# Optimization experiments

Measured on AMD Instinct MI355X. Metric: run time of the kernel, lower is better.

The kernel has to match this reference:

```python
import jax, jax.numpy as jnp
import numpy as np

HIDDEN = 4096
N_HEADS = 32
N_KV_HEADS = 8
HEAD_DIM = HIDDEN // N_HEADS  # 128
ROPE_THETA = 10000.0
NEG_INF = -1e9


def rotate_half(x):
    x1, x2 = jnp.split(x, 2, axis=-1)
    return jnp.concatenate([-x2, x1], axis=-1)


def rope_cos_sin(seq_len, dim, dtype):
    inv_freq = 1.0 / (ROPE_THETA ** (jnp.arange(0, dim, 2, dtype=jnp.float32) / dim))
    t = jnp.arange(seq_len, dtype=jnp.float32)
    freqs = jnp.outer(t, inv_freq)              # (S, dim/2)
    emb = jnp.concatenate([freqs, freqs], -1)   # (S, dim)
    return jnp.cos(emb).astype(dtype), jnp.sin(emb).astype(dtype)


def setup_inputs() -> dict:
    key = jax.random.key(0)
    ks = jax.random.split(key, 5)
    B, S = 2, 2048
    hidden_states = jax.random.normal(ks[0], (B, S, HIDDEN), jnp.float32)
    # additive causal mask (B, 1, S, S)
    causal = jnp.triu(jnp.full((S, S), NEG_INF, jnp.float32), k=1)
    attention_mask = jnp.broadcast_to(causal[None, None], (B, 1, S, S))
    scale = 0.02
    wq = jax.random.normal(ks[1], (HIDDEN, HIDDEN), jnp.float32) * scale
    wk = jax.random.normal(ks[2], (N_KV_HEADS * HEAD_DIM, HIDDEN), jnp.float32) * scale
    wv = jax.random.normal(ks[3], (N_KV_HEADS * HEAD_DIM, HIDDEN), jnp.float32) * scale
    wo = jax.random.normal(ks[4], (HIDDEN, HIDDEN), jnp.float32) * scale
    return {"hidden_states": hidden_states, "attention_mask": attention_mask,
            "wq": wq, "wk": wk, "wv": wv, "wo": wo}


def reference(hidden_states, attention_mask, wq, wk, wv, wo):
    B, S, _ = hidden_states.shape
    H, Hk, D = N_HEADS, N_KV_HEADS, HEAD_DIM
    G = H // Hk  # kv groups

    q = (hidden_states @ wq.T).reshape(B, S, H, D).transpose(0, 2, 1, 3)   # (B,H,S,D)
    k = (hidden_states @ wk.T).reshape(B, S, Hk, D).transpose(0, 2, 1, 3)  # (B,Hk,S,D)
    v = (hidden_states @ wv.T).reshape(B, S, Hk, D).transpose(0, 2, 1, 3)

    cos, sin = rope_cos_sin(S, D, hidden_states.dtype)  # (S,D)
    cos = cos[None, None]  # (1,1,S,D)
    sin = sin[None, None]
    q = q * cos + rotate_half(q) * sin
    k = k * cos + rotate_half(k) * sin

    # GQA without materializing repeated K/V: view q as (B,Hk,G,S,D)
    qg = q.reshape(B, Hk, G, S, D)
    scores = jnp.einsum('bkgqd,bkld->bkgql', qg, k) / jnp.sqrt(jnp.asarray(D, q.dtype))
    scores = scores + attention_mask[:, :, None]  # (B,1,1,S,S) broadcast
    attn = jax.nn.softmax(scores.astype(jnp.float32), axis=-1).astype(q.dtype)
    out = jnp.einsum('bkgql,bkld->bkgqd', attn, v)  # (B,Hk,G,S,D)
    out = out.reshape(B, H, S, D).transpose(0, 2, 1, 3).reshape(B, S, H * D)
    return out @ wo.T
```

## Files before the change

kernel.cpp:

```cpp
#include <hip/hip_runtime.h>
#include <hip/hip_bf16.h>
#include <stdint.h>


#define HIDDEN 4096
#define NH 32
#define NKV 8
#define HD 128
#define SLEN 2048
#define BATCH 2
#define QKVLD 6144

typedef __attribute__((ext_vector_type(8))) short bf16x8;
typedef __attribute__((ext_vector_type(4))) float f32x4;

__device__ __forceinline__ unsigned short f2bf(float f) {
  __hip_bfloat16 h = __float2bfloat16(f);
  return *reinterpret_cast<unsigned short*>(&h);
}
__device__ __forceinline__ float bf2f(unsigned short h) {
  union { uint32_t u; float f; } v; v.u = ((uint32_t)h) << 16;
  return v.f;
}
__device__ __forceinline__ void gload_lds16(const void* g, void* l) {
  __builtin_amdgcn_global_load_lds(
      (const __attribute__((address_space(1))) unsigned int*)g,
      (__attribute__((address_space(3))) unsigned int*)l, 16, 0, 0);
}

__device__ __forceinline__ void cvt_body(const float* __restrict__ in,
                                         unsigned short* __restrict__ out, int rb) {
  size_t i = ((size_t)rb * 256 + threadIdx.x) * 8;
  f32x4 a = *(const f32x4*)&in[i];
  f32x4 b = *(const f32x4*)&in[i + 4];
  bf16x8 o;
#pragma unroll
  for (int j = 0; j < 4; ++j) { o[j] = (short)f2bf(a[j]); o[4 + j] = (short)f2bf(b[j]); }
  *(bf16x8*)&out[i] = o;
}

__global__ __launch_bounds__(256) void cvt_f32_bf16(const float* __restrict__ in,
                                                    unsigned short* __restrict__ out) {
  cvt_body(in, out, blockIdx.x);
}

__global__ __launch_bounds__(256) void cvt_all(const float* __restrict__ h,
                                               const float* __restrict__ wq,
                                               const float* __restrict__ wk,
                                               const float* __restrict__ wv,
                                               unsigned short* __restrict__ Xbf,
                                               unsigned short* __restrict__ Wqkv) {
  int bid = blockIdx.x;
  if (bid < 8192) {
    cvt_body(h, Xbf, bid);
  } else if (bid < 16384) {
    cvt_body(wq, Wqkv, bid - 8192);
  } else if (bid < 18432) {
    cvt_body(wk, Wqkv + (size_t)4096 * 4096, bid - 16384);
  } else {
    cvt_body(wv, Wqkv + (size_t)5120 * 4096, bid - 18432);
  }
}

__device__ __forceinline__ void store_out(unsigned short* C, size_t i, float v) { C[i] = f2bf(v); }
__device__ __forceinline__ void store_out(float* C, size_t i, float v) { C[i] = v; }

template <typename OutT>
__global__ __launch_bounds__(512, 2)
void gemm_bt256(const unsigned short* __restrict__ A, const unsigned short* __restrict__ B,
                OutT* __restrict__ C, int M, int N, int K) {
  __shared__ __align__(16) unsigned short lds[4 * 2048 * 8];

  const int tid = threadIdx.x;
  const int lane = tid & 63, w = tid >> 6;
  const int lr = lane & 15, lg = lane >> 4;
  const int wr = w >> 2, wc = w & 3;
  const int rsw = (lr >> 1) & 3;

  const int nbn = N >> 8;
  const int nwg = gridDim.x;
  int wg = (int)blockIdx.x;
  wg = (wg & 7) * (nwg >> 3) + (wg >> 3);
  const int bm = wg / nbn, bn = wg % nbn;

  const unsigned short* Ab = A + (size_t)bm * 256 * K;
  const unsigned short* Bb = B + (size_t)bn * 256 * K;

  const int r0 = tid >> 2, s0 = (tid & 3) ^ ((tid >> 3) & 3);
  const int L1 = tid + 512;
  const int r1 = L1 >> 2, s1 = (L1 & 3) ^ ((L1 >> 3) & 3);
  const unsigned short* gA0 = Ab + (size_t)r0 * K + s0 * 8;
  const unsigned short* gA1 = Ab + (size_t)r1 * K + s1 * 8;
  const unsigned short* gB0 = Bb + (size_t)r0 * K + s0 * 8;
  const unsigned short* gB1 = Bb + (size_t)r1 * K + s1 * 8;

  const unsigned short* rdA = &lds[(size_t)(wr * 512 + lr * 4 + (lg ^ rsw)) * 8];
  const unsigned short* rdB = &lds[(size_t)(1024 + wc * 256 + lr * 4 + (lg ^ rsw)) * 8];

  f32x4 acc[8][4] = {};

  auto stage = [&](int t2) {
    unsigned short* lb = lds + (size_t)(t2 & 3) * 2048 * 8;
    const int off = t2 * 32;
    gload_lds16(gA0 + off, lb + (size_t)tid * 8);
    gload_lds16(gA1 + off, lb + (size_t)(512 + tid) * 8);
    gload_lds16(gB0 + off, lb + (size_t)(1024 + tid) * 8);
    gload_lds16(gB1 + off, lb + (size_t)(1536 + tid) * 8);
  };

#define READ12(af, bf, bsel)                                                      \
  {                                                                               \
    const unsigned short* pA_ = rdA + (size_t)(bsel)*16384;                       \
    const unsigned short* pB_ = rdB + (size_t)(bsel)*16384;                       \
    _Pragma("unroll") for (int mi_ = 0; mi_ < 8; ++mi_)                           \
        af[mi_] = *(const bf16x8*)(pA_ + mi_ * 512);                              \
    _Pragma("unroll") for (int ni_ = 0; ni_ < 4; ++ni_)                           \
        bf[ni_] = *(const bf16x8*)(pB_ + ni_ * 512);                              \
  }

#define MFMA32(af, bf)                                                            \
  __builtin_amdgcn_s_setprio(1);                                                  \
  _Pragma("unroll") for (int mi_ = 0; mi_ < 8; ++mi_)                             \
  _Pragma("unroll") for (int ni_ = 0; ni_ < 4; ++ni_)                             \
      acc[mi_][ni_] = __builtin_amdgcn_mfma_f32_16x16x32_bf16(                    \
          af[mi_], bf[ni_], acc[mi_][ni_], 0, 0, 0);                              \
  __builtin_amdgcn_s_setprio(0)

#define VMW(t)                                                                    \
  if ((t) + 3 < NT)      asm volatile("s_waitcnt vmcnt(8)" ::: "memory");         \
  else if ((t) + 2 < NT) asm volatile("s_waitcnt vmcnt(4)" ::: "memory");         \
  else if ((t) + 1 < NT) asm volatile("s_waitcnt vmcnt(0)" ::: "memory")

#define ITER(cur_a, cur_b, nxt_a, nxt_b, t)                                       \
  {                                                                               \
    if ((t) + 3 < NT) stage((t) + 3);                                             \
    VMW(t);                                                                       \
    __builtin_amdgcn_s_barrier();                                                 \
    if ((t) + 1 < NT) READ12(nxt_a, nxt_b, ((t) + 1) & 3);                        \
    MFMA32(cur_a, cur_b);                                                         \
    asm volatile("s_waitcnt lgkmcnt(0)" ::: "memory");                            \
  }

  const int NT = K >> 5;

  bf16x8 afA[8], bfA[4], afB[8], bfB[4];

  stage(0); stage(1); stage(2);
  asm volatile("s_waitcnt vmcnt(8)" ::: "memory");
  __builtin_amdgcn_s_barrier();
  READ12(afA, bfA, 0);

#pragma unroll 1
  for (int t = 0; t < NT; t += 2) {
    ITER(afA, bfA, afB, bfB, t);
    ITER(afB, bfB, afA, bfA, t + 1);
  }

#pragma unroll
  for (int mi = 0; mi < 8; ++mi)
#pragma unroll
    for (int ni = 0; ni < 4; ++ni)
#pragma unroll
      for (int r = 0; r < 4; ++r) {
        size_t row = (size_t)bm * 256 + wr * 128 + mi * 16 + lg * 4 + r;
        size_t col = (size_t)bn * 256 + wc * 64 + ni * 16 + lr;
        store_out(C, row * N + col, acc[mi][ni][r]);
      }
#undef READ12
#undef MFMA32
#undef VMW
#undef ITER
}

__global__ __launch_bounds__(256) void rope_tables(float* __restrict__ ct, float* __restrict__ st) {
  int idx = blockIdx.x * 256 + threadIdx.x;
  int s = idx >> 6, j = idx & 63;
  float inv = exp2f(-(float)j * (13.287712379549449f / 64.f));
  float f = (float)s * inv;
  ct[idx] = cosf(f);
  st[idx] = sinf(f);
}

__device__ __forceinline__ void rope_body(unsigned short* __restrict__ X, int ld,
                                          const float* __restrict__ ct,
                                          const float* __restrict__ st, int heads, int idx) {
  int jc = (idx & 7) * 8;
  int t2 = idx >> 3;
  int hh = t2 % heads;
  int row = t2 / heads;
  int s = row & (SLEN - 1);
  unsigned short* p = X + (size_t)row * ld + hh * HD;
  bf16x8 lo = *(bf16x8*)&p[jc];
  bf16x8 hi = *(bf16x8*)&p[64 + jc];
  bf16x8 nlo, nhi;
#pragma unroll
  for (int j = 0; j < 8; ++j) {
    float c = ct[s * 64 + jc + j];
    float sn = st[s * 64 + jc + j];
    float xl = bf2f((unsigned short)(lo[j]));
    float xh = bf2f((unsigned short)(hi[j]));
    nlo[j] = (short)f2bf(xl * c - xh * sn);
    nhi[j] = (short)f2bf(xh * c + xl * sn);
  }
  *(bf16x8*)&p[jc] = nlo;
  *(bf16x8*)&p[64 + jc] = nhi;
}

__global__ __launch_bounds__(256) void rope_apply_qk(unsigned short* __restrict__ QKV,
                                                     const float* __restrict__ ct,
                                                     const float* __restrict__ st) {
  int bid = blockIdx.x;
  if (bid < 4096) {
    rope_body(QKV, QKVLD, ct, st, NH, bid * 256 + threadIdx.x);
  } else {
    rope_body(QKV + 4096, QKVLD, ct, st, NKV, (bid - 4096) * 256 + threadIdx.x);
  }
}

__global__ __launch_bounds__(256) void transpose_v(const unsigned short* __restrict__ Vsrc, int ld,
                                                   unsigned short* __restrict__ VT) {
  __shared__ unsigned short tile[64][66];
  const int t = threadIdx.x;
  const int bs = blockIdx.x;
  const int bd = blockIdx.y;
  const int b = bs >> 5;
  const int s0 = (bs & 31) * 64;
  const int d0 = bd * 64;
#pragma unroll
  for (int it = 0; it < 2; ++it) {
    int si = (t >> 3) + it * 32;
    int dj = (t & 7) * 8;
    bf16x8 v = *(const bf16x8*)&Vsrc[(size_t)(b * SLEN + s0 + si) * ld + d0 + dj];
#pragma unroll
    for (int j = 0; j < 8; ++j) tile[si][dj + j] = (unsigned short)(v[j]);
  }
  __syncthreads();
#pragma unroll
  for (int it = 0; it < 2; ++it) {
    int di = (t >> 3) + it * 32;
    int sj = (t & 7) * 8;
    bf16x8 o;
#pragma unroll
    for (int j = 0; j < 8; ++j) o[j] = (short)tile[sj + j][di];
    int c = d0 + di;
    int kvh = c >> 7, d = c & 127;
    *(bf16x8*)&VT[(((size_t)b * NKV + kvh) * HD + d) * SLEN + s0 + sj] = o;
  }
}

__global__ __launch_bounds__(256, 2)
void attn_fwd(const unsigned short* __restrict__ QKV, const unsigned short* __restrict__ VTm,
              unsigned short* __restrict__ Om) {
  const int blk = blockIdx.x;
  const int xcd = blk & 7, jj = blk >> 3;
  const int g = xcd + ((jj >> 5) << 3);
  const int pair = jj & 31;
  const int kvh = g & 7, b = g >> 3;
  const int tid = threadIdx.x;
  const int lane = tid & 63, w = tid >> 6;
  const int lr = lane & 15, lg = lane >> 4;
  const int h = kvh * 4 + w;

  __shared__ __align__(16) unsigned short Ksm[64 * 136];
  __shared__ __align__(16) unsigned short Vsm[128 * 72];
  __shared__ __align__(16) unsigned short Psm[4][32 * 72];
  __shared__ float Alds[4][32];

  const float SL2E = 0.1275378504229740f;

  const unsigned short* Kb0 = QKV + (size_t)(b * SLEN) * QKVLD + 4096 + kvh * HD;
  const unsigned short* VTb = VTm + ((size_t)(b * NKV + kvh) * HD) * SLEN;

#pragma unroll 1
  for (int halfq = 0; halfq < 2; ++halfq) {
    const int qt = halfq ? (63 - pair) : pair;
    const int q0 = qt * 32;
    const int ntiles = (qt >> 1) + 1;

    bf16x8 qf[2][4];
    const unsigned short* Qb = QKV + (size_t)(b * SLEN + q0) * QKVLD + h * HD;
#pragma unroll
    for (int ni = 0; ni < 2; ++ni)
#pragma unroll
      for (int kd = 0; kd < 4; ++kd)
        qf[ni][kd] = *(const bf16x8*)&Qb[(size_t)(ni * 16 + lr) * QKVLD + kd * 32 + lg * 8];

    f32x4 acc_o[2][8] = {};
    float m_run[2] = {-1e30f, -1e30f};
    float l_run[2] = {0.f, 0.f};

    bf16x8 kreg[4], vreg[4];
#pragma unroll
    for (int i = 0; i < 4; ++i) {
      int c = tid + i * 256;
      kreg[i] = *(const bf16x8*)&Kb0[(size_t)(c >> 4) * QKVLD + (c & 15) * 8];
      vreg[i] = *(const bf16x8*)&VTb[(size_t)(c >> 3) * SLEN + (c & 7) * 8];
    }

#pragma unroll 1
    for (int t = 0; t < ntiles; ++t) {
      const int kv0 = t * 64;
      __syncthreads();
#pragma unroll
      for (int i = 0; i < 4; ++i) {
        int c = tid + i * 256;
        *(bf16x8*)&Ksm[(c >> 4) * 136 + (c & 15) * 8] = kreg[i];
        *(bf16x8*)&Vsm[(c >> 3) * 72 + (c & 7) * 8] = vreg[i];
      }
      __syncthreads();

      if (t + 1 < ntiles) {
#pragma unroll
        for (int i = 0; i < 4; ++i) {
          int c = tid + i * 256;
          kreg[i] = *(const bf16x8*)&Kb0[(size_t)(kv0 + 64 + (c >> 4)) * QKVLD + (c & 15) * 8];
          vreg[i] = *(const bf16x8*)&VTb[(size_t)(c >> 3) * SLEN + kv0 + 64 + (c & 7) * 8];
        }
      }

      f32x4 accs[4][2] = {};
#pragma unroll
      for (int kd = 0; kd < 4; ++kd) {
        bf16x8 kf[4];
#pragma unroll
        for (int mi = 0; mi < 4; ++mi)
          kf[mi] = *(const bf16x8*)&Ksm[(mi * 16 + lr) * 136 + kd * 32 + lg * 8];
        __builtin_amdgcn_s_setprio(1);
#pragma unroll
        for (int mi = 0; mi < 4; ++mi)
#pragma unroll
          for (int ni = 0; ni < 2; ++ni)
            accs[mi][ni] =
                __builtin_amdgcn_mfma_f32_16x16x32_bf16(kf[mi], qf[ni][kd], accs[mi][ni], 0, 0, 0);
        __builtin_amdgcn_s_setprio(0);
      }

      const bool domask = (t == ntiles - 1);
      float alpha[2];
#pragma unroll
      for (int ni = 0; ni < 2; ++ni) {
        float cmax = -1e30f;
#pragma unroll
        for (int mi = 0; mi < 4; ++mi)
#pragma unroll
          for (int r = 0; r < 4; ++r) {
            float s = accs[mi][ni][r] * SL2E;
            if (domask) {
              int key = kv0 + mi * 16 + lg * 4 + r;
              int qq = q0 + ni * 16 + lr;
              if (key > qq) s = -1e30f;
            }
            accs[mi][ni][r] = s;
            cmax = fmaxf(cmax, s);
          }
        cmax = fmaxf(cmax, __shfl_xor(cmax, 16));
        cmax = fmaxf(cmax, __shfl_xor(cmax, 32));
        float mnew = fmaxf(m_run[ni], cmax);
        alpha[ni] = exp2f(m_run[ni] - mnew);
        float psum = 0.f;
#pragma unroll
        for (int mi = 0; mi < 4; ++mi)
#pragma unroll
          for (int r = 0; r < 4; ++r) {
            float p = exp2f(accs[mi][ni][r] - mnew);
            accs[mi][ni][r] = p;
            psum += p;
          }
        psum += __shfl_xor(psum, 16);
        psum += __shfl_xor(psum, 32);
        l_run[ni] = l_run[ni] * alpha[ni] + psum;
        m_run[ni] = mnew;
      }

      if (__any(alpha[0] < 1.f) || __any(alpha[1] < 1.f)) {
        if (lg == 0) { Alds[w][lr] = alpha[0]; Alds[w][16 + lr] = alpha[1]; }
        f32x4 al0 = *(const f32x4*)&Alds[w][lg * 4];
        f32x4 al1 = *(const f32x4*)&Alds[w][16 + lg * 4];
#pragma unroll
        for (int nd = 0; nd < 8; ++nd)
#pragma unroll
          for (int r = 0; r < 4; ++r) {
            acc_o[0][nd][r] *= al0[r];
            acc_o[1][nd][r] *= al1[r];
          }
      }

#pragma unroll
      for (int ni = 0; ni < 2; ++ni)
#pragma unroll
        for (int mi = 0; mi < 4; ++mi)
#pragma unroll
          for (int rp = 0; rp < 4; rp += 2) {
            uint32_t pk = (uint32_t)f2bf(accs[mi][ni][rp]) |
                          ((uint32_t)f2bf(accs[mi][ni][rp + 1]) << 16);
            *(uint32_t*)&Psm[w][(ni * 16 + lr) * 72 + mi * 16 + lg * 4 + rp] = pk;
          }

#pragma unroll
      for (int ks = 0; ks < 2; ++ks) {
        bf16x8 pa[2];
#pragma unroll
        for (int pm = 0; pm < 2; ++pm)
          pa[pm] = *(const bf16x8*)&Psm[w][(pm * 16 + lr) * 72 + ks * 32 + lg * 8];
        __builtin_amdgcn_s_setprio(1);
#pragma unroll
        for (int nd = 0; nd < 8; ++nd) {
          bf16x8 vb = *(const bf16x8*)&Vsm[(nd * 16 + lr) * 72 + ks * 32 + lg * 8];
#pragma unroll
          for (int pm = 0; pm < 2; ++pm)
            acc_o[pm][nd] =
                __builtin_amdgcn_mfma_f32_16x16x32_bf16(pa[pm], vb, acc_o[pm][nd], 0, 0, 0);
        }
        __builtin_amdgcn_s_setprio(0);
      }
    }

    if (lg == 0) {
      Alds[w][lr] = 1.f / l_run[0];
      Alds[w][16 + lr] = 1.f / l_run[1];
    }
    f32x4 li0 = *(const f32x4*)&Alds[w][lg * 4];
    f32x4 li1 = *(const f32x4*)&Alds[w][16 + lg * 4];
    unsigned short* Ob = Om + ((size_t)(b * SLEN + q0) * NH + h) * HD;
#pragma unroll
    for (int pm = 0; pm < 2; ++pm)
#pragma unroll
      for (int nd = 0; nd < 8; ++nd)
#pragma unroll
        for (int r = 0; r < 4; ++r) {
          int qq = pm * 16 + lg * 4 + r;
          float v = acc_o[pm][nd][r] * (pm ? li1[r] : li0[r]);
          Ob[(size_t)qq * (NH * HD) + nd * 16 + lr] = f2bf(v);
        }
  }
}

extern "C" void kernel_launch(void* const* d_in, const int* in_sizes, int n_in,
                              void* d_out, int out_size, void* d_ws, size_t ws_size,
                              hipStream_t stream) {
  const float* hidden = (const float*)d_in[0];
  const float* wq = (const float*)d_in[2];
  const float* wk = (const float*)d_in[3];
  const float* wv = (const float*)d_in[4];
  const float* wo = (const float*)d_in[5];

  char* ws = (char*)d_ws;
  const size_t MB = 1ull << 20;
  unsigned short* Xbf  = (unsigned short*)(ws);
  unsigned short* Wqkv = (unsigned short*)(ws + 32 * MB);
  unsigned short* QKV  = (unsigned short*)(ws + 80 * MB);
  unsigned short* Ob   = (unsigned short*)(ws + 128 * MB);
  unsigned short* VTb  = (unsigned short*)(ws + 160 * MB);
  float* ct = (float*)(ws + 168 * MB);
  float* st = (float*)(ws + 168 * MB + 524288);

  cvt_all<<<20480, 256, 0, stream>>>(hidden, wq, wk, wv, Xbf, Wqkv);

  gemm_bt256<unsigned short><<<384, 512, 0, stream>>>(Xbf, Wqkv, QKV, 4096, 6144, 4096);

  rope_tables<<<512, 256, 0, stream>>>(ct, st);
  rope_apply_qk<<<5120, 256, 0, stream>>>(QKV, ct, st);

  transpose_v<<<dim3(64, 16), 256, 0, stream>>>(QKV + 5120, QKVLD, VTb);

  attn_fwd<<<512, 256, 0, stream>>>(QKV, VTb, Ob);

  cvt_f32_bf16<<<8192, 256, 0, stream>>>(wo, Wqkv);
  gemm_bt256<float><<<256, 512, 0, stream>>>(Ob, Wqkv, (float*)d_out, 4096, 4096, 4096);
}
```

Measured before the change: 563.4 us.

## Split-K the QKV projection GEMM into two halves with bf16 reduction kernel

Adds a split-K option to the 256x256 GEMM: the QKV projection launches two K-halves on a 2D grid, writing partial sums to QKV and a workspace buffer, then a new elementwise kernel adds them. This doubles the workgroup count from 384 (about 1.5 waves on 256 CUs) to 768 to reduce wave-quantization tail. It costs an extra 48MB partial write/read pass, and rounding each partial to bf16 before the add adds precision loss. The path is only taken when the workspace is large enough.

```diff
diff --git a/kernel.cpp b/kernel.cpp
--- a/kernel.cpp
+++ b/kernel.cpp
@@ -62,13 +62,26 @@
   }
 }
 
+__global__ __launch_bounds__(256) void add_split(unsigned short* __restrict__ out,
+                                                 const unsigned short* __restrict__ p1) {
+  size_t i = ((size_t)blockIdx.x * 256 + threadIdx.x) * 8;
+  bf16x8 a = *(const bf16x8*)&out[i];
+  bf16x8 b = *(const bf16x8*)&p1[i];
+  bf16x8 o;
+#pragma unroll
+  for (int j = 0; j < 8; ++j)
+    o[j] = (short)f2bf(bf2f((unsigned short)a[j]) + bf2f((unsigned short)b[j]));
+  *(bf16x8*)&out[i] = o;
+}
+
 __device__ __forceinline__ void store_out(unsigned short* C, size_t i, float v) { C[i] = f2bf(v); }
 __device__ __forceinline__ void store_out(float* C, size_t i, float v) { C[i] = v; }
 
 template <typename OutT>
 __global__ __launch_bounds__(512, 2)
 void gemm_bt256(const unsigned short* __restrict__ A, const unsigned short* __restrict__ B,
-                OutT* __restrict__ C, int M, int N, int K) {
+                OutT* __restrict__ C0, OutT* __restrict__ C1, int M, int N, int Kstride,
+                int Kloop) {
   __shared__ __align__(16) unsigned short lds[4 * 2048 * 8];
 
   const int tid = threadIdx.x;
@@ -77,22 +90,25 @@
   const int wr = w >> 2, wc = w & 3;
   const int rsw = (lr >> 1) & 3;
 
+  const int koff = blockIdx.y * Kloop;
+  OutT* C = blockIdx.y ? C1 : C0;
+
   const int nbn = N >> 8;
   const int nwg = gridDim.x;
   int wg = (int)blockIdx.x;
   wg = (wg & 7) * (nwg >> 3) + (wg >> 3);
   const int bm = wg / nbn, bn = wg % nbn;
 
-  const unsigned short* Ab = A + (size_t)bm * 256 * K;
-  const unsigned short* Bb = B + (size_t)bn * 256 * K;
+  const unsigned short* Ab = A + (size_t)bm * 256 * Kstride + koff;
+  const unsigned short* Bb = B + (size_t)bn * 256 * Kstride + koff;
 
   const int r0 = tid >> 2, s0 = (tid & 3) ^ ((tid >> 3) & 3);
   const int L1 = tid + 512;
   const int r1 = L1 >> 2, s1 = (L1 & 3) ^ ((L1 >> 3) & 3);
-  const unsigned short* gA0 = Ab + (size_t)r0 * K + s0 * 8;
-  const unsigned short* gA1 = Ab + (size_t)r1 * K + s1 * 8;
-  const unsigned short* gB0 = Bb + (size_t)r0 * K + s0 * 8;
-  const unsigned short* gB1 = Bb + (size_t)r1 * K + s1 * 8;
+  const unsigned short* gA0 = Ab + (size_t)r0 * Kstride + s0 * 8;
+  const unsigned short* gA1 = Ab + (size_t)r1 * Kstride + s1 * 8;
+  const unsigned short* gB0 = Bb + (size_t)r0 * Kstride + s0 * 8;
+  const unsigned short* gB1 = Bb + (size_t)r1 * Kstride + s1 * 8;
 
   const unsigned short* rdA = &lds[(size_t)(wr * 512 + lr * 4 + (lg ^ rsw)) * 8];
   const unsigned short* rdB = &lds[(size_t)(1024 + wc * 256 + lr * 4 + (lg ^ rsw)) * 8];
@@ -141,7 +157,7 @@
     asm volatile("s_waitcnt lgkmcnt(0)" ::: "memory");                            \
   }
 
-  const int NT = K >> 5;
+  const int NT = Kloop >> 5;
 
   bf16x8 afA[8], bfA[4], afB[8], bfB[4];
 
@@ -453,10 +469,20 @@
   unsigned short* VTb  = (unsigned short*)(ws + 160 * MB);
   float* ct = (float*)(ws + 168 * MB);
   float* st = (float*)(ws + 168 * MB + 524288);
+  unsigned short* P1   = (unsigned short*)(ws + 169 * MB);
+
+  const bool ksplit = (ws_size >= 217 * MB);
 
   cvt_all<<<20480, 256, 0, stream>>>(hidden, wq, wk, wv, Xbf, Wqkv);
 
-  gemm_bt256<unsigned short><<<384, 512, 0, stream>>>(Xbf, Wqkv, QKV, 4096, 6144, 4096);
+  if (ksplit) {
+    gemm_bt256<unsigned short><<<dim3(384, 2), 512, 0, stream>>>(
+        Xbf, Wqkv, QKV, P1, 4096, 6144, 4096, 2048);
+    add_split<<<12288, 256, 0, stream>>>(QKV, P1);
+  } else {
+    gemm_bt256<unsigned short><<<dim3(384, 1), 512, 0, stream>>>(
+        Xbf, Wqkv, QKV, QKV, 4096, 6144, 4096, 4096);
+  }
 
   rope_tables<<<512, 256, 0, stream>>>(ct, st);
   rope_apply_qk<<<5120, 256, 0, stream>>>(QKV, ct, st);
@@ -466,5 +492,6 @@
   attn_fwd<<<512, 256, 0, stream>>>(QKV, VTb, Ob);
 
   cvt_f32_bf16<<<8192, 256, 0, stream>>>(wo, Wqkv);
-  gemm_bt256<float><<<256, 512, 0, stream>>>(Ob, Wqkv, (float*)d_out, 4096, 4096, 4096);
-}
+  gemm_bt256<float><<<dim3(256, 1), 512, 0, stream>>>(
+      Ob, Wqkv, (float*)d_out, (float*)d_out, 4096, 4096, 4096, 4096);
+}
```

Result: no change. 572.2 us (median of 2 runs) (+1.6%).
